# Kernel tuning notes

Hardware: AMD Instinct MI355X
Metric: run time of the kernel (lower is better)

## Reference

```python
import jax, jax.numpy as jnp
import numpy as np

D_MODEL = 1024
NUM_HEADS = 16
D_K = D_MODEL // NUM_HEADS
ROPE_THETA = 10000.0


def apply_rope(x, positions):
    # x: (b, h, s, d_k), positions: (b, s) int
    half = D_K // 2
    inv_freq = ROPE_THETA ** (-jnp.arange(half, dtype=jnp.float32) * 2.0 / D_K)  # (half,)
    angles = positions[:, None, :, None].astype(jnp.float32) * inv_freq  # (b,1,s,half)
    cos, sin = jnp.cos(angles), jnp.sin(angles)
    x_even = x[..., 0::2]
    x_odd = x[..., 1::2]
    r_even = x_even * cos - x_odd * sin
    r_odd = x_even * sin + x_odd * cos
    # re-interleave
    out = jnp.stack([r_even, r_odd], axis=-1).reshape(x.shape)
    return out


def setup_inputs() -> dict:
    key = jax.random.key(0)
    k1, k2, k3, k4, k5 = jax.random.split(key, 5)
    b, s = 2, 2048
    scale = 1.0 / np.sqrt(D_MODEL)
    x = jax.random.normal(k1, (b, s, D_MODEL), dtype=jnp.float32)
    w_q = jax.random.normal(k2, (D_MODEL, D_MODEL), dtype=jnp.float32) * scale
    w_k = jax.random.normal(k3, (D_MODEL, D_MODEL), dtype=jnp.float32) * scale
    w_v = jax.random.normal(k4, (D_MODEL, D_MODEL), dtype=jnp.float32) * scale
    w_o = jax.random.normal(k5, (D_MODEL, D_MODEL), dtype=jnp.float32) * scale
    token_positions = jnp.broadcast_to(jnp.arange(s, dtype=jnp.int64 if jax.config.jax_enable_x64 else jnp.int32), (b, s))
    return {"x": x, "w_q": w_q, "w_k": w_k, "w_v": w_v, "w_o": w_o,
            "token_positions": token_positions}


def reference(x, w_q, w_k, w_v, w_o, token_positions):
    b, s, _ = x.shape
    # QKV projections: w_* are (h*d_k, d_model); y = x @ w^T
    def proj(w):
        y = jnp.einsum('bsd,ed->bse', x, w)  # (b,s,h*d_k)
        return y.reshape(b, s, NUM_HEADS, D_K).transpose(0, 2, 1, 3)  # (b,h,s,d_k)
    Q, K, V = proj(w_q), proj(w_k), proj(w_v)
    Q = apply_rope(Q, token_positions)
    K = apply_rope(K, token_positions)
    scores = jnp.einsum('bhqd,bhkd->bhqk', Q, K) / jnp.sqrt(jnp.float32(D_K))
    causal = jnp.tril(jnp.ones((s, s), dtype=bool))
    scores = jnp.where(causal[None, None], scores, -jnp.inf)
    attn = jax.nn.softmax(scores, axis=-1)
    out = jnp.einsum('bhqk,bhkd->bhqd', attn, V)  # (b,h,s,d_v)
    out = out.transpose(0, 2, 1, 3).reshape(b, s, NUM_HEADS * D_K)
    return jnp.einsum('bse,de->bsd', out, w_o)
```

## Files before the change

kernel.cpp:

```cpp
#include <hip/hip_runtime.h>

#define B_ 2
#define S_ 2048
#define DM 1024
#define NH 16
#define DK 64

using bf16x8  = __attribute__((ext_vector_type(8)))  short;
using f32x4   = __attribute__((ext_vector_type(4)))  float;

__device__ __forceinline__ float bf2f(short v){
  unsigned u = ((unsigned)(unsigned short)v) << 16;
  union { unsigned u; float f; } c; c.u = u; return c.f;
}
__device__ __forceinline__ short f2bf(float f){
  union { float f; unsigned u; } c; c.f = f;
  unsigned u = c.u + 0x7FFFu + ((c.u >> 16) & 1u);
  return (short)(u >> 16);
}
__device__ __forceinline__ unsigned packbf(float lo, float hi){
  union { float f; unsigned u; } a, b; a.f = lo; b.f = hi;
  return __builtin_amdgcn_perm(b.u, a.u, 0x07060302u);
}
__device__ __forceinline__ void gload16(const void* g, void* l){
  __builtin_amdgcn_global_load_lds(
    (const __attribute__((address_space(1))) unsigned*)g,
    (__attribute__((address_space(3))) unsigned*)l, 16, 0, 0);
}

__global__ void rope_table(const int* __restrict__ pos, float* __restrict__ tab){
  int idx = blockIdx.x * blockDim.x + threadIdx.x;
  if (idx >= B_ * S_ * 32) return;
  int j = idx & 31, bs = idx >> 5;
  float p = (float)pos[bs];
  float inv = powf(10000.0f, -(float)(2 * j) / 64.0f);
  float ang = p * inv;
  tab[(size_t)bs * 64 + j]      = cosf(ang);
  tab[(size_t)bs * 64 + 32 + j] = sinf(ang);
}

__global__ void cast_all(const float* __restrict__ x, const float* __restrict__ wq,
                         const float* __restrict__ wk, const float* __restrict__ wv,
                         const float* __restrict__ wo,
                         short* __restrict__ xb, short* __restrict__ wqkv,
                         short* __restrict__ wob){
  int i = blockIdx.x * blockDim.x + threadIdx.x;
  const float4* src; short4* dst;
  if (i < (1 << 20)){
    src = (const float4*)x + i; dst = (short4*)xb + i;
  } else {
    int j = i - (1 << 20);
    int seg = j >> 18, off = j & ((1 << 18) - 1);
    const float* sp = seg == 0 ? wq : seg == 1 ? wk : seg == 2 ? wv : wo;
    short* dp = seg < 3 ? wqkv + ((size_t)seg << 20) : wob;
    src = (const float4*)sp + off; dst = (short4*)dp + off;
  }
  float4 v = *src;
  short4 o; o.x = f2bf(v.x); o.y = f2bf(v.y); o.z = f2bf(v.z); o.w = f2bf(v.w);
  *dst = o;
}

__launch_bounds__(512)
__global__ void gemm_qkv(const short* __restrict__ A, const short* __restrict__ Bm,
                         const float* __restrict__ tab,
                         short* __restrict__ Qr, short* __restrict__ Kr,
                         short* __restrict__ Vq, int K){
  __shared__ short As[128 * 32];
  __shared__ short Bs[128 * 32];
  const int tid = threadIdx.x;
  const int l = tid & 63, w = tid >> 6;
  const int lr = l & 15, lg = l >> 4;
  const int wr = w >> 2, wc = w & 3;
  const int nwg = gridDim.x * gridDim.y;
  const int wg  = blockIdx.y * gridDim.x + blockIdx.x;
  const int sw  = (wg & 7) * (nwg >> 3) + (wg >> 3);
  const int bn  = sw % gridDim.x, bm = sw / gridDim.x;
  const short* Ab = A + (size_t)bm * 128 * K;
  const short* Bb = Bm + (size_t)bn * 128 * K;
  f32x4 acc[4][2];
  #pragma unroll
  for (int m = 0; m < 4; ++m)
    #pragma unroll
    for (int n = 0; n < 2; ++n) acc[m][n] = (f32x4){0.f, 0.f, 0.f, 0.f};
  const int r0 = tid >> 2, q4 = tid & 3;
  for (int kt = 0; kt < K; kt += 32){
    gload16(Ab + (size_t)r0 * K + kt + q4 * 8, As + tid * 8);
    gload16(Bb + (size_t)r0 * K + kt + q4 * 8, Bs + tid * 8);
    __syncthreads();
    bf16x8 a[4], bfr[2];
    #pragma unroll
    for (int m = 0; m < 4; ++m)
      a[m] = *(const bf16x8*)(As + (wr * 64 + m * 16 + lr) * 32 + lg * 8);
    #pragma unroll
    for (int n = 0; n < 2; ++n)
      bfr[n] = *(const bf16x8*)(Bs + (wc * 32 + n * 16 + lr) * 32 + lg * 8);
    #pragma unroll
    for (int m = 0; m < 4; ++m)
      #pragma unroll
      for (int n = 0; n < 2; ++n)
        acc[m][n] = __builtin_amdgcn_mfma_f32_16x16x32_bf16(a[m], bfr[n], acc[m][n], 0, 0, 0);
    __syncthreads();
  }
  #pragma unroll
  for (int m = 0; m < 4; ++m)
    #pragma unroll
    for (int n = 0; n < 2; ++n){
      const int col = bn * 128 + wc * 32 + n * 16 + lr;
      const int which = col >> 10;
      #pragma unroll
      for (int j = 0; j < 4; ++j){
        const int row = bm * 128 + wr * 64 + m * 16 + lg * 4 + j;
        float v = acc[m][n][j];
        if (which == 2){
          Vq[(size_t)row * 1024 + (col - 2048)] = f2bf(v);
        } else {
          const int d  = col & 63;
          const int dp = d >> 1;
          const float c = tab[(size_t)row * 64 + dp];
          const float s = tab[(size_t)row * 64 + 32 + dp];
          const float p = __shfl_xor(v, 1);
          float r = v * c + p * ((d & 1) ? s : -s);
          if (which == 0) r *= 0.125f;
          short* dst = which ? Kr : Qr;
          const int b = row >> 11, si = row & 2047;
          const int h = (col >> 6) & 15;
          dst[(((size_t)(b * NH + h)) * S_ + si) * DK + d] = f2bf(r);
        }
      }
    }
}

template<typename OutT>
__launch_bounds__(512)
__global__ void gemm_bt8(const short* __restrict__ A, const short* __restrict__ Bm,
                         OutT* __restrict__ C, int M, int N, int K){
  __shared__ short As[128 * 32];
  __shared__ short Bs[128 * 32];
  const int tid = threadIdx.x;
  const int l = tid & 63, w = tid >> 6;
  const int lr = l & 15, lg = l >> 4;
  const int wr = w >> 2, wc = w & 3;
  const int nwg = gridDim.x * gridDim.y;
  const int wg  = blockIdx.y * gridDim.x + blockIdx.x;
  const int sw  = (wg & 7) * (nwg >> 3) + (wg >> 3);
  const int bn  = sw % gridDim.x, bm = sw / gridDim.x;
  const short* Ab = A + (size_t)bm * 128 * K;
  const short* Bb = Bm + (size_t)bn * 128 * K;
  f32x4 acc[4][2];
  #pragma unroll
  for (int m = 0; m < 4; ++m)
    #pragma unroll
    for (int n = 0; n < 2; ++n) acc[m][n] = (f32x4){0.f, 0.f, 0.f, 0.f};
  const int r0 = tid >> 2, q4 = tid & 3;
  for (int kt = 0; kt < K; kt += 32){
    gload16(Ab + (size_t)r0 * K + kt + q4 * 8, As + tid * 8);
    gload16(Bb + (size_t)r0 * K + kt + q4 * 8, Bs + tid * 8);
    __syncthreads();
    bf16x8 a[4], bfr[2];
    #pragma unroll
    for (int m = 0; m < 4; ++m)
      a[m] = *(const bf16x8*)(As + (wr * 64 + m * 16 + lr) * 32 + lg * 8);
    #pragma unroll
    for (int n = 0; n < 2; ++n)
      bfr[n] = *(const bf16x8*)(Bs + (wc * 32 + n * 16 + lr) * 32 + lg * 8);
    #pragma unroll
    for (int m = 0; m < 4; ++m)
      #pragma unroll
      for (int n = 0; n < 2; ++n)
        acc[m][n] = __builtin_amdgcn_mfma_f32_16x16x32_bf16(a[m], bfr[n], acc[m][n], 0, 0, 0);
    __syncthreads();
  }
  #pragma unroll
  for (int m = 0; m < 4; ++m)
    #pragma unroll
    for (int n = 0; n < 2; ++n)
      #pragma unroll
      for (int j = 0; j < 4; ++j){
        int row = bm * 128 + wr * 64 + m * 16 + lg * 4 + j;
        int col = bn * 128 + wc * 32 + n * 16 + lr;
        float v = acc[m][n][j];
        if constexpr (__is_same(OutT, short)) C[(size_t)row * N + col] = f2bf(v);
        else                                  C[(size_t)row * N + col] = v;
      }
}

__global__ void vtrans(const short* __restrict__ Vq, short* __restrict__ Vt){
  __shared__ short t[64][72];
  const int tid = threadIdx.x;
  const int st = blockIdx.x, bh = blockIdx.y;
  const int b = bh >> 4, h = bh & 15;
  #pragma unroll
  for (int i = 0; i < 2; ++i){
    int c = tid + 256 * i;
    int sl = c >> 3, d8 = c & 7;
    const short* src = Vq + ((size_t)b * S_ + st * 64 + sl) * 1024 + h * 64 + d8 * 8;
    *(bf16x8*)(&t[sl][d8 * 8]) = *(const bf16x8*)src;
  }
  __syncthreads();
  #pragma unroll
  for (int i = 0; i < 2; ++i){
    int c = tid + 256 * i;
    int dl = c >> 3, s8 = c & 7;
    bf16x8 v;
    #pragma unroll
    for (int jj = 0; jj < 8; ++jj) v[jj] = t[s8 * 8 + jj][dl];
    short* dst = Vt + ((size_t)bh * DK + dl) * S_ + st * 64 + s8 * 8;
    *(bf16x8*)dst = v;
  }
}

__device__ __forceinline__ void attn_tile_step(
    const bf16x8 qa0, const bf16x8 qa1,
    f32x4 (&acc)[4], float& mrow, float& lsum,
    const short* Ks, const short* Vs, unsigned* pw,
    int diagmask, int lr, int lg, int wl){
  float sv[4][4];
  #pragma unroll
  for (int n = 0; n < 4; ++n){
    const int R = n * 16 + lr;
    const int c0 = lg ^ (R & 7);
    bf16x8 k0 = *(const bf16x8*)(Ks + R * 64 + c0 * 8);
    bf16x8 k1 = *(const bf16x8*)(Ks + R * 64 + (c0 ^ 4) * 8);
    f32x4 z = (f32x4){0.f, 0.f, 0.f, 0.f};
    z = __builtin_amdgcn_mfma_f32_16x16x32_bf16(k0, qa0, z, 0, 0, 0);
    z = __builtin_amdgcn_mfma_f32_16x16x32_bf16(k1, qa1, z, 0, 0, 0);
    #pragma unroll
    for (int j = 0; j < 4; ++j) sv[n][j] = z[j];
  }
  if (diagmask){
    const int qloc = wl * 16 + lr;
    #pragma unroll
    for (int n = 0; n < 4; ++n)
      #pragma unroll
      for (int j = 0; j < 4; ++j)
        if (n * 16 + lg * 4 + j > qloc) sv[n][j] = -1e30f;
  }
  float lm = sv[0][0];
  #pragma unroll
  for (int n = 0; n < 4; ++n)
    #pragma unroll
    for (int j = 0; j < 4; ++j) lm = fmaxf(lm, sv[n][j]);
  lm = fmaxf(lm, __shfl_xor(lm, 16));
  lm = fmaxf(lm, __shfl_xor(lm, 32));
  if (!__all(lm <= mrow + 8.f)){
    float mnew = fmaxf(mrow, lm);
    float corr = __expf(mrow - mnew);
    mrow = mnew;
    lsum *= corr;
    float cb[4];
    #pragma unroll
    for (int j = 0; j < 4; ++j) cb[j] = __shfl(corr, lg * 4 + j);
    #pragma unroll
    for (int n = 0; n < 4; ++n)
      #pragma unroll
      for (int j = 0; j < 4; ++j) acc[n][j] *= cb[j];
  }
  float psum = 0.f;
  #pragma unroll
  for (int n = 0; n < 4; ++n)
    #pragma unroll
    for (int j = 0; j < 4; ++j){
      float p = __expf(sv[n][j] - mrow);
      sv[n][j] = p; psum += p;
    }
  psum += __shfl_xor(psum, 16);
  psum += __shfl_xor(psum, 32);
  lsum += psum;
  const int swz = (lr & 7) << 2;
  #pragma unroll
  for (int n = 0; n < 4; ++n){
    pw[lr * 32 + ((n * 8 + lg * 2 + 0) ^ swz)] = packbf(sv[n][0], sv[n][1]);
    pw[lr * 32 + ((n * 8 + lg * 2 + 1) ^ swz)] = packbf(sv[n][2], sv[n][3]);
  }
  bf16x8 pa0 = *(const bf16x8*)(pw + lr * 32 + ((lg * 4) ^ swz));
  bf16x8 pa1 = *(const bf16x8*)(pw + lr * 32 + ((16 + lg * 4) ^ swz));
  #pragma unroll
  for (int n = 0; n < 4; ++n){
    const int R = n * 16 + lr;
    const int c0 = lg ^ (R & 7);
    bf16x8 v0 = *(const bf16x8*)(Vs + R * 64 + c0 * 8);
    bf16x8 v1 = *(const bf16x8*)(Vs + R * 64 + (c0 ^ 4) * 8);
    acc[n] = __builtin_amdgcn_mfma_f32_16x16x32_bf16(pa0, v0, acc[n], 0, 0, 0);
    acc[n] = __builtin_amdgcn_mfma_f32_16x16x32_bf16(pa1, v1, acc[n], 0, 0, 0);
  }
}

__launch_bounds__(512)
__global__ void attn_kernel(const short* __restrict__ Qr, const short* __restrict__ Kr,
                            const short* __restrict__ Vt, short* __restrict__ AO){
  __shared__ short Ks[2][64 * 64];
  __shared__ short Vs[2][64 * 64];
  __shared__ unsigned Pw[8][16 * 32];
  const int tid = threadIdx.x;
  const int l = tid & 63, w = tid >> 6;
  const int lr = l & 15, lg = l >> 4;
  const int wl = w & 3, wgp = w >> 2;
  const int qp = blockIdx.x, h = blockIdx.y, b = blockIdx.z;
  const int t0 = qp, t1 = 31 - qp;
  const int myqt = wgp ? t0 : t1;
  const int bh = b * NH + h;
  const short* Qp = Qr + (size_t)bh * S_ * DK;
  const short* Kp = Kr + (size_t)bh * S_ * DK;
  const short* Vp = Vt + (size_t)bh * DK * S_;

  bf16x8 qa0, qa1;
  {
    const short* q0 = Qp + (size_t)(myqt * 64 + wl * 16 + lr) * DK + lg * 8;
    qa0 = *(const bf16x8*)q0; qa1 = *(const bf16x8*)(q0 + 32);
  }
  f32x4 acc[4];
  float ms = -1e30f, ls = 0.f;
  #pragma unroll
  for (int n = 0; n < 4; ++n) acc[n] = (f32x4){0.f, 0.f, 0.f, 0.f};
  unsigned* pw = &Pw[w][0];
  const int r0 = tid >> 3, q8 = tid & 7;
  const int sq8 = q8 ^ (r0 & 7);

  gload16(Kp + (size_t)r0 * DK + sq8 * 8, &Ks[0][tid * 8]);
  gload16(Vp + (size_t)r0 * S_ + sq8 * 8, &Vs[0][tid * 8]);
  int cur = 0;
  for (int kt = 0; kt <= t1; ++kt){
    __syncthreads();
    if (kt < t1){
      gload16(Kp + (size_t)((kt + 1) * 64 + r0) * DK + sq8 * 8, &Ks[cur ^ 1][tid * 8]);
      gload16(Vp + (size_t)r0 * S_ + (kt + 1) * 64 + sq8 * 8,   &Vs[cur ^ 1][tid * 8]);
    }
    if (kt <= myqt)
      attn_tile_step(qa0, qa1, acc, ms, ls, Ks[cur], Vs[cur], pw, kt == myqt, lr, lg, wl);
    cur ^= 1;
  }
  const float li = 1.f / ls;
  #pragma unroll
  for (int j = 0; j < 4; ++j){
    const float d0 = __shfl(li, lg * 4 + j);
    #pragma unroll
    for (int n = 0; n < 4; ++n){
      int e = h * 64 + n * 16 + lr;
      int r = myqt * 64 + wl * 16 + lg * 4 + j;
      AO[((size_t)b * S_ + r) * DM + e] = f2bf(acc[n][j] * d0);
    }
  }
}

extern "C" void kernel_launch(void* const* d_in, const int* in_sizes, int n_in,
                              void* d_out, int out_size, void* d_ws, size_t ws_size,
                              hipStream_t stream){
  const float* x  = (const float*)d_in[0];
  const float* wq = (const float*)d_in[1];
  const float* wk = (const float*)d_in[2];
  const float* wv = (const float*)d_in[3];
  const float* wo = (const float*)d_in[4];
  const int*  pos = (const int*)d_in[5];

  char* ws = (char*)d_ws;
  short* xb   = (short*)(ws + 0);
  short* wqkv = (short*)(ws + ((size_t)8  << 20));
  short* wob  = (short*)(ws + ((size_t)14 << 20));
  short* Vq   = (short*)(ws + ((size_t)16 << 20));
  short* Qr   = (short*)(ws + ((size_t)40 << 20));
  short* Kr   = (short*)(ws + ((size_t)48 << 20));
  short* Vt   = (short*)(ws + ((size_t)56 << 20));
  float* tab  = (float*)(ws + ((size_t)64 << 20));
  short* AO   = xb;
  float* out  = (float*)d_out;

  rope_table<<<dim3((B_ * S_ * 32 + 255) / 256), dim3(256), 0, stream>>>(pos, tab);
  cast_all<<<dim3(8192), dim3(256), 0, stream>>>(x, wq, wk, wv, wo, xb, wqkv, wob);
  gemm_qkv<<<dim3(24, 32), dim3(512), 0, stream>>>(xb, wqkv, tab, Qr, Kr, Vq, 1024);
  vtrans<<<dim3(32, 32), dim3(256), 0, stream>>>(Vq, Vt);
  attn_kernel<<<dim3(16, NH, B_), dim3(512), 0, stream>>>(Qr, Kr, Vt, AO);
  gemm_bt8<float><<<dim3(8, 32), dim3(512), 0, stream>>>(AO, wob, out, 4096, 1024, 1024);
}
```

Before: 130.9 us.

## Rewrite QKV GEMM with 256x256 tiles and 4-stage LDS pipeline

Replaces the 128x128 QKV projection GEMM with a 256x256-tile version that keeps a four-deep ring of LDS buffers. Global loads for the next three k-steps are issued while the current step runs MFMAs, with explicit vmcnt waits in place of two barriers per step. MFMA priority is raised during the compute phase. The aim is to hide global-load latency and increase register-level reuse. In exchange it needs 128KB of dynamic LDS and many more accumulator registers, and the grid drops to 192 workgroups, which may underfill the GPU.

Result: slower. 147.9 us (+13.0%).

```diff
diff --git a/kernel.cpp b/kernel.cpp
--- a/kernel.cpp
+++ b/kernel.cpp
@@ -60,56 +60,77 @@
   *dst = o;
 }
 
-__launch_bounds__(512)
-__global__ void gemm_qkv(const short* __restrict__ A, const short* __restrict__ Bm,
-                         const float* __restrict__ tab,
-                         short* __restrict__ Qr, short* __restrict__ Kr,
-                         short* __restrict__ Vq, int K){
-  __shared__ short As[128 * 32];
-  __shared__ short Bs[128 * 32];
+__launch_bounds__(512, 2)
+__global__ void gemm_qkv2(const short* __restrict__ A, const short* __restrict__ Bm,
+                          const float* __restrict__ tab,
+                          short* __restrict__ Qr, short* __restrict__ Kr,
+                          short* __restrict__ Vq){
+  extern __shared__ short lds[];
+  constexpr int K = 1024, NT = 32;
   const int tid = threadIdx.x;
-  const int l = tid & 63, w = tid >> 6;
+  const int l = tid & 63, wid = tid >> 6;
   const int lr = l & 15, lg = l >> 4;
-  const int wr = w >> 2, wc = w & 3;
+  const int wr = wid >> 2, wc = wid & 3;
   const int nwg = gridDim.x * gridDim.y;
   const int wg  = blockIdx.y * gridDim.x + blockIdx.x;
   const int sw  = (wg & 7) * (nwg >> 3) + (wg >> 3);
   const int bn  = sw % gridDim.x, bm = sw / gridDim.x;
-  const short* Ab = A + (size_t)bm * 128 * K;
-  const short* Bb = Bm + (size_t)bn * 128 * K;
-  f32x4 acc[4][2];
-  #pragma unroll
-  for (int m = 0; m < 4; ++m)
-    #pragma unroll
-    for (int n = 0; n < 2; ++n) acc[m][n] = (f32x4){0.f, 0.f, 0.f, 0.f};
-  const int r0 = tid >> 2, q4 = tid & 3;
-  for (int kt = 0; kt < K; kt += 32){
-    gload16(Ab + (size_t)r0 * K + kt + q4 * 8, As + tid * 8);
-    gload16(Bb + (size_t)r0 * K + kt + q4 * 8, Bs + tid * 8);
-    __syncthreads();
-    bf16x8 a[4], bfr[2];
-    #pragma unroll
-    for (int m = 0; m < 4; ++m)
-      a[m] = *(const bf16x8*)(As + (wr * 64 + m * 16 + lr) * 32 + lg * 8);
-    #pragma unroll
-    for (int n = 0; n < 2; ++n)
-      bfr[n] = *(const bf16x8*)(Bs + (wc * 32 + n * 16 + lr) * 32 + lg * 8);
-    #pragma unroll
-    for (int m = 0; m < 4; ++m)
-      #pragma unroll
-      for (int n = 0; n < 2; ++n)
-        acc[m][n] = __builtin_amdgcn_mfma_f32_16x16x32_bf16(a[m], bfr[n], acc[m][n], 0, 0, 0);
-    __syncthreads();
-  }
-  #pragma unroll
-  for (int m = 0; m < 4; ++m)
-    #pragma unroll
-    for (int n = 0; n < 2; ++n){
-      const int col = bn * 128 + wc * 32 + n * 16 + lr;
-      const int which = col >> 10;
+  const short* Ab = A  + (size_t)bm * 256 * K;
+  const short* Bb = Bm + (size_t)bn * 256 * K;
+  const int r0 = tid >> 2, c4 = tid & 3;
+
+  f32x4 acc[8][4];
+  #pragma unroll
+  for (int m = 0; m < 8; ++m)
+    #pragma unroll
+    for (int n = 0; n < 4; ++n) acc[m][n] = (f32x4){0.f, 0.f, 0.f, 0.f};
+
+  auto stage = [&](int t){
+    short* buf = lds + (size_t)(t & 3) * 16384;
+    const short* ab = Ab + (size_t)r0 * K + t * 32 + c4 * 8;
+    gload16(ab,                   buf + tid * 8);
+    gload16(ab + (size_t)128 * K, buf + (tid + 512) * 8);
+    const short* bb = Bb + (size_t)r0 * K + t * 32 + c4 * 8;
+    gload16(bb,                   buf + 8192 + tid * 8);
+    gload16(bb + (size_t)128 * K, buf + 8192 + (tid + 512) * 8);
+  };
+
+  stage(0); stage(1); stage(2);
+  for (int t = 0; t < NT; ++t){
+    if (t < NT - 2)      asm volatile("s_waitcnt vmcnt(8)" ::: "memory");
+    else if (t == NT-2)  asm volatile("s_waitcnt vmcnt(4)" ::: "memory");
+    else                 asm volatile("s_waitcnt vmcnt(0)" ::: "memory");
+    __builtin_amdgcn_s_barrier();
+    __builtin_amdgcn_sched_barrier(0);
+    if (t + 3 < NT) stage(t + 3);
+    const short* bufA = lds + (size_t)(t & 3) * 16384;
+    const short* bufB = bufA + 8192;
+    bf16x8 af[8], bfr[4];
+    #pragma unroll
+    for (int m = 0; m < 8; ++m)
+      af[m] = *(const bf16x8*)(bufA + (wr * 128 + m * 16 + lr) * 32 + lg * 8);
+    #pragma unroll
+    for (int n = 0; n < 4; ++n)
+      bfr[n] = *(const bf16x8*)(bufB + (wc * 64 + n * 16 + lr) * 32 + lg * 8);
+    __builtin_amdgcn_s_setprio(1);
+    #pragma unroll
+    for (int m = 0; m < 8; ++m)
+      #pragma unroll
+      for (int n = 0; n < 4; ++n)
+        acc[m][n] = __builtin_amdgcn_mfma_f32_16x16x32_bf16(af[m], bfr[n], acc[m][n], 0, 0, 0);
+    __builtin_amdgcn_s_setprio(0);
+  }
+
+  const int colb = bn * 256 + wc * 64;
+  #pragma unroll
+  for (int n = 0; n < 4; ++n){
+    const int col = colb + n * 16 + lr;
+    const int which = col >> 10;
+    #pragma unroll
+    for (int m = 0; m < 8; ++m)
       #pragma unroll
       for (int j = 0; j < 4; ++j){
-        const int row = bm * 128 + wr * 64 + m * 16 + lg * 4 + j;
+        const int row = bm * 256 + wr * 128 + m * 16 + lg * 4 + j;
         float v = acc[m][n][j];
         if (which == 2){
           Vq[(size_t)row * 1024 + (col - 2048)] = f2bf(v);
@@ -127,7 +148,7 @@
           dst[(((size_t)(b * NH + h)) * S_ + si) * DK + d] = f2bf(r);
         }
       }
-    }
+  }
 }
 
 template<typename OutT>
@@ -364,9 +385,11 @@
   short* AO   = xb;
   float* out  = (float*)d_out;
 
+  hipFuncSetAttribute((const void*)gemm_qkv2, hipFuncAttributeMaxDynamicSharedMemorySize, 131072);
+
   rope_table<<<dim3((B_ * S_ * 32 + 255) / 256), dim3(256), 0, stream>>>(pos, tab);
   cast_all<<<dim3(8192), dim3(256), 0, stream>>>(x, wq, wk, wv, wo, xb, wqkv, wob);
-  gemm_qkv<<<dim3(24, 32), dim3(512), 0, stream>>>(xb, wqkv, tab, Qr, Kr, Vq, 1024);
+  gemm_qkv2<<<dim3(12, 16), dim3(512), 131072, stream>>>(xb, wqkv, tab, Qr, Kr, Vq);
   vtrans<<<dim3(32, 32), dim3(256), 0, stream>>>(Vq, Vt);
   attn_kernel<<<dim3(16, NH, B_), dim3(512), 0, stream>>>(Qr, Kr, Vt, AO);
   gemm_bt8<float><<<dim3(8, 32), dim3(512), 0, stream>>>(AO, wob, out, 4096, 1024, 1024);
```
